# Performance work log

Hardware: AMD Instinct MI355X
Metric: run time of the kernel (lower is better)

## Reference

```python
import jax, jax.numpy as jnp
import numpy as np

EMB = 512
N_MODELS = 5
HID = 64
N_Q = 2048
N_P = 256


def setup_inputs() -> dict:
    key = jax.random.key(0)
    ks = jax.random.split(key, 6)
    return {
        "query_features": jax.random.normal(ks[0], (N_Q, EMB), dtype=jnp.float32),
        "prototypes": jax.random.normal(ks[1], (N_P, EMB), dtype=jnp.float32),
        # first Linear: weight [64, 2*EMB], bias [64], per model
        "W1": jax.random.normal(ks[2], (N_MODELS, HID, 2 * EMB), dtype=jnp.float32) * 0.02,
        "b1": jax.random.normal(ks[3], (N_MODELS, HID), dtype=jnp.float32) * 0.02,
        # second Linear: weight [1, 64] -> stored as [64], bias scalar per model
        "W2": jax.random.normal(ks[4], (N_MODELS, HID), dtype=jnp.float32) * 0.02,
        "b2": jax.random.normal(ks[5], (N_MODELS,), dtype=jnp.float32) * 0.02,
    }


def reference(query_features, prototypes, W1, b1, W2, b2):
    d = query_features.shape[1]
    # cat([q_i, p_j]) @ W1^T == q_i @ W1[:, :d]^T + p_j @ W1[:, d:]^T
    W1q = W1[:, :, :d]   # [M, H, d]
    W1p = W1[:, :, d:]   # [M, H, d]
    hq = jnp.einsum('qd,mhd->mqh', query_features, W1q)  # [M, Q, H]
    hp = jnp.einsum('pd,mhd->mph', prototypes, W1p)      # [M, P, H]
    h = jax.nn.relu(hq[:, :, None, :] + hp[:, None, :, :] + b1[:, None, None, :])  # [M, Q, P, H]
    out = jnp.einsum('mqph,mh->mqp', h, W2) + b2[:, None, None]  # [M, Q, P]
    mean_d = out.mean(axis=0)
    # torch.std default is unbiased (ddof=1)
    unc = jnp.std(out, axis=0, ddof=1)
    return mean_d * jnp.exp(-unc)
```

## Files before the change

### kernel.cpp

```cpp
#include <hip/hip_runtime.h>
#include <math.h>

#define EMB 512
#define NM 5
#define HID 64
#define NQ 2048
#define NP 256

typedef __attribute__((ext_vector_type(8))) short short8;
typedef __attribute__((ext_vector_type(4))) float floatx4;

#define A_BY 0u
#define B_BY 2621440u

#define LST 72

__device__ inline unsigned short bfr(float f) {
    unsigned u = __float_as_uint(f);
    u += 0x7FFFu + ((u >> 16) & 1u);
    return (unsigned short)(u >> 16);
}

__device__ inline void cvt8(float4 a, float4 b, short8& hi, short8& lo) {
#define C1(I, V) { unsigned short h_ = bfr(V); hi[I] = (short)h_; \
    lo[I] = (short)bfr(V - __uint_as_float(((unsigned)h_) << 16)); }
    C1(0, a.x) C1(1, a.y) C1(2, a.z) C1(3, a.w)
    C1(4, b.x) C1(5, b.y) C1(6, b.z) C1(7, b.w)
#undef C1
}
__device__ inline void cvt8hi(float4 a, float4 b, short8& hi) {
    hi[0] = (short)bfr(a.x); hi[1] = (short)bfr(a.y);
    hi[2] = (short)bfr(a.z); hi[3] = (short)bfr(a.w);
    hi[4] = (short)bfr(b.x); hi[5] = (short)bfr(b.y);
    hi[6] = (short)bfr(b.z); hi[7] = (short)bfr(b.w);
}

__global__ __launch_bounds__(256) void gemm_v3(const float* __restrict__ Q,
                                               const float* __restrict__ P,
                                               const float* __restrict__ W1,
                                               const float* __restrict__ b1,
                                               float* __restrict__ A,
                                               float* __restrict__ Bv) {
    __shared__ short XH[2][16 * LST];
    __shared__ short WH[2][64 * LST];
    __shared__ short WL[2][64 * LST];

    int tid  = threadIdx.x;
    int lane = tid & 63;
    int ht   = tid >> 6;
    int m    = blockIdx.x % 5;
    int rt   = blockIdx.x / 5;
    int r0   = rt * 16;
    bool isQ = rt < 128;

    int wrow = tid >> 3;
    int wg8  = (tid & 7) * 8;
    const float* wb  = W1 + (size_t)m * 64 * 1024 + (isQ ? 0 : EMB);
    const float* wp0 = wb + (size_t)wrow * 1024 + wg8;
    const float* wp1 = wb + (size_t)(wrow + 32) * 1024 + wg8;
    bool hasX = tid < 128;
    int xrow  = tid >> 3;
    const float* xp = (isQ ? Q + (size_t)(r0 + xrow) * EMB
                           : P + (size_t)(r0 - NQ + xrow) * EMB) + wg8;

    int arix = (lane & 15) * LST + (lane >> 4) * 8;
    int brix = (ht * 16 + (lane & 15)) * LST + (lane >> 4) * 8;

    floatx4 ac = {0, 0, 0, 0};
    float4 w00, w01, w10, w11, x0, x1;

    w00 = *(const float4*)&wp0[0]; w01 = *(const float4*)&wp0[4];
    w10 = *(const float4*)&wp1[0]; w11 = *(const float4*)&wp1[4];
    if (hasX) { x0 = *(const float4*)&xp[0]; x1 = *(const float4*)&xp[4]; }
    {
        short8 hi, lo;
        cvt8(w00, w01, hi, lo);
        *(short8*)&WH[0][wrow * LST + wg8] = hi;
        *(short8*)&WL[0][wrow * LST + wg8] = lo;
        cvt8(w10, w11, hi, lo);
        *(short8*)&WH[0][(wrow + 32) * LST + wg8] = hi;
        *(short8*)&WL[0][(wrow + 32) * LST + wg8] = lo;
        if (hasX) { short8 xh; cvt8hi(x0, x1, xh);
                    *(short8*)&XH[0][xrow * LST + wg8] = xh; }
    }

#pragma unroll 1
    for (int c = 0; c < 8; ++c) {
        int cur = c & 1;
        if (c < 7) {
            int k0 = (c + 1) * 64;
            w00 = *(const float4*)&wp0[k0]; w01 = *(const float4*)&wp0[k0 + 4];
            w10 = *(const float4*)&wp1[k0]; w11 = *(const float4*)&wp1[k0 + 4];
            if (hasX) { x0 = *(const float4*)&xp[k0]; x1 = *(const float4*)&xp[k0 + 4]; }
        }
        __syncthreads();

#pragma unroll
        for (int s = 0; s < 2; ++s) {
            short8 Ah = *(const short8*)&XH[cur][arix + s * 32];
            short8 Bh = *(const short8*)&WH[cur][brix + s * 32];
            short8 Bl = *(const short8*)&WL[cur][brix + s * 32];
            ac = __builtin_amdgcn_mfma_f32_16x16x32_bf16(Ah, Bl, ac, 0, 0, 0);
            ac = __builtin_amdgcn_mfma_f32_16x16x32_bf16(Ah, Bh, ac, 0, 0, 0);
        }

        if (c < 7) {
            int nb = cur ^ 1;
            short8 hi, lo;
            cvt8(w00, w01, hi, lo);
            *(short8*)&WH[nb][wrow * LST + wg8] = hi;
            *(short8*)&WL[nb][wrow * LST + wg8] = lo;
            cvt8(w10, w11, hi, lo);
            *(short8*)&WH[nb][(wrow + 32) * LST + wg8] = hi;
            *(short8*)&WL[nb][(wrow + 32) * LST + wg8] = lo;
            if (hasX) { short8 xh; cvt8hi(x0, x1, xh);
                        *(short8*)&XH[nb][xrow * LST + wg8] = xh; }
        }
    }

    int col  = lane & 15;
    int rloc = (lane >> 4) * 4;
    int hh   = ht * 16 + col;
    int rr   = r0 + rloc;

    if (isQ) {
        float bb = b1[m * 64 + hh];
        float* dst = &A[((size_t)m * NQ + rr) * HID + hh];
        dst[0 * HID] = ac.x + bb; dst[1 * HID] = ac.y + bb;
        dst[2 * HID] = ac.z + bb; dst[3 * HID] = ac.w + bb;
    } else {
        int p = rr - NQ;
        float* dst = &Bv[(((size_t)(m * 16 + (hh >> 2))) * NP + p) * 4 + (hh & 3)];
        dst[0 * 4] = ac.x; dst[1 * 4] = ac.y; dst[2 * 4] = ac.z; dst[3 * 4] = ac.w;
    }
}

__global__ __launch_bounds__(256) void fused_main(const float* __restrict__ A,
                                                  const float* __restrict__ Bv,
                                                  const float* __restrict__ W2,
                                                  const float* __restrict__ b2,
                                                  float* __restrict__ out) {
    int p  = threadIdx.x;
    int q0 = blockIdx.x * 2;

    float s1a = 0, s2a = 0, s1b = 0, s2b = 0;
    const float4* Bq = (const float4*)Bv + p;

#pragma unroll 1
    for (int m = 0; m < NM; ++m) {
        const float4* bm = Bq + (size_t)m * 16 * NP;
        float4 B0 = bm[0*NP],  B1 = bm[1*NP],  B2 = bm[2*NP],  B3 = bm[3*NP];
        float4 B4 = bm[4*NP],  B5 = bm[5*NP],  B6 = bm[6*NP],  B7 = bm[7*NP];
        float4 B8 = bm[8*NP],  B9 = bm[9*NP],  B10= bm[10*NP], B11= bm[11*NP];
        float4 B12= bm[12*NP], B13= bm[13*NP], B14= bm[14*NP], B15= bm[15*NP];

        const float* Ar  = A + ((size_t)m * NQ + q0) * HID;
        const float* Wp2 = W2 + m * HID;
        float oa = 0.f, ob = 0.f;

#define HSTEP(BF, H0) { \
        float wa=Wp2[H0+0], wb=Wp2[H0+1], wc=Wp2[H0+2], wd=Wp2[H0+3]; \
        oa = fmaf(fmaxf(Ar[H0+0]    + BF.x, 0.f), wa, oa); \
        oa = fmaf(fmaxf(Ar[H0+1]    + BF.y, 0.f), wb, oa); \
        oa = fmaf(fmaxf(Ar[H0+2]    + BF.z, 0.f), wc, oa); \
        oa = fmaf(fmaxf(Ar[H0+3]    + BF.w, 0.f), wd, oa); \
        ob = fmaf(fmaxf(Ar[64+H0+0] + BF.x, 0.f), wa, ob); \
        ob = fmaf(fmaxf(Ar[64+H0+1] + BF.y, 0.f), wb, ob); \
        ob = fmaf(fmaxf(Ar[64+H0+2] + BF.z, 0.f), wc, ob); \
        ob = fmaf(fmaxf(Ar[64+H0+3] + BF.w, 0.f), wd, ob); }

        HSTEP(B0,  0)  HSTEP(B1,  4)  HSTEP(B2,  8)  HSTEP(B3, 12)
        HSTEP(B4, 16)  HSTEP(B5, 20)  HSTEP(B6, 24)  HSTEP(B7, 28)
        HSTEP(B8, 32)  HSTEP(B9, 36)  HSTEP(B10,40)  HSTEP(B11,44)
        HSTEP(B12,48)  HSTEP(B13,52)  HSTEP(B14,56)  HSTEP(B15,60)
#undef HSTEP

        float bb = b2[m];
        float xa = oa + bb, xb = ob + bb;
        s1a += xa; s2a = fmaf(xa, xa, s2a);
        s1b += xb; s2b = fmaf(xb, xb, s2b);
    }

    {
        float mean = s1a * 0.2f;
        float var  = fmaxf((s2a - s1a * s1a * 0.2f) * 0.25f, 0.f);
        out[(size_t)q0 * NP + p] = mean * __expf(-sqrtf(var));
    }
    {
        float mean = s1b * 0.2f;
        float var  = fmaxf((s2b - s1b * s1b * 0.2f) * 0.25f, 0.f);
        out[(size_t)(q0 + 1) * NP + p] = mean * __expf(-sqrtf(var));
    }
}

extern "C" void kernel_launch(void* const* d_in, const int* in_sizes, int n_in,
                              void* d_out, int out_size, void* d_ws, size_t ws_size,
                              hipStream_t stream) {
    const float* Q  = (const float*)d_in[0];
    const float* P  = (const float*)d_in[1];
    const float* W1 = (const float*)d_in[2];
    const float* b1 = (const float*)d_in[3];
    const float* W2 = (const float*)d_in[4];
    const float* b2 = (const float*)d_in[5];
    float* out = (float*)d_out;

    char*  ws = (char*)d_ws;
    float* A  = (float*)(ws + A_BY);
    float* B  = (float*)(ws + B_BY);

    gemm_v3<<<720, 256, 0, stream>>>(Q, P, W1, b1, A, B);
    fused_main<<<1024, 256, 0, stream>>>(A, B, W2, b2, out);
}
```

Before: 93.16 us.

## Split projection GEMM into single-wave blocks to drop block-level barriers

The projection GEMM now launches 2880 blocks of one 64-thread wavefront each, every block computing one 16x16 output tile instead of a 16x64 tile shared by four waves. Because each block is a single wave, the __syncthreads in the double-buffered K loop is removed. The goal is to cut barrier stalls and spread the work over more blocks. The cost is that each query/prototype row tile is now loaded and converted to bf16 four times instead of once, so global loads and conversion work rise.

Result: slower. 100.1 us (+7.4%).

```diff
diff --git a/kernel.cpp b/kernel.cpp
--- a/kernel.cpp
+++ b/kernel.cpp
@@ -35,53 +35,52 @@
     hi[6] = (short)bfr(b.z); hi[7] = (short)bfr(b.w);
 }
 
-__global__ __launch_bounds__(256) void gemm_v3(const float* __restrict__ Q,
-                                               const float* __restrict__ P,
-                                               const float* __restrict__ W1,
-                                               const float* __restrict__ b1,
-                                               float* __restrict__ A,
-                                               float* __restrict__ Bv) {
+__global__ __launch_bounds__(64) void gemm_w(const float* __restrict__ Q,
+                                             const float* __restrict__ P,
+                                             const float* __restrict__ W1,
+                                             const float* __restrict__ b1,
+                                             float* __restrict__ A,
+                                             float* __restrict__ Bv) {
     __shared__ short XH[2][16 * LST];
-    __shared__ short WH[2][64 * LST];
-    __shared__ short WL[2][64 * LST];
-
-    int tid  = threadIdx.x;
-    int lane = tid & 63;
-    int ht   = tid >> 6;
-    int m    = blockIdx.x % 5;
-    int rt   = blockIdx.x / 5;
+    __shared__ short WH[2][16 * LST];
+    __shared__ short WL[2][16 * LST];
+
+    int lane = threadIdx.x;
+    int b    = blockIdx.x;
+    int ht   = b & 3;
+    int mr   = b >> 2;
+    int m    = mr % 5;
+    int rt   = mr / 5;
     int r0   = rt * 16;
     bool isQ = rt < 128;
 
-    int wrow = tid >> 3;
-    int wg8  = (tid & 7) * 8;
-    const float* wb  = W1 + (size_t)m * 64 * 1024 + (isQ ? 0 : EMB);
-    const float* wp0 = wb + (size_t)wrow * 1024 + wg8;
-    const float* wp1 = wb + (size_t)(wrow + 32) * 1024 + wg8;
-    bool hasX = tid < 128;
-    int xrow  = tid >> 3;
-    const float* xp = (isQ ? Q + (size_t)(r0 + xrow) * EMB
-                           : P + (size_t)(r0 - NQ + xrow) * EMB) + wg8;
+    int srow = lane >> 2;
+    int sk   = (lane & 3) * 16;
+    const float* xp = (isQ ? Q + (size_t)(r0 + srow) * EMB
+                           : P + (size_t)(r0 - NQ + srow) * EMB) + sk;
+    const float* wp = W1 + ((size_t)m * 64 + ht * 16 + srow) * 1024
+                      + (isQ ? 0 : EMB) + sk;
 
     int arix = (lane & 15) * LST + (lane >> 4) * 8;
-    int brix = (ht * 16 + (lane & 15)) * LST + (lane >> 4) * 8;
 
     floatx4 ac = {0, 0, 0, 0};
-    float4 w00, w01, w10, w11, x0, x1;
-
-    w00 = *(const float4*)&wp0[0]; w01 = *(const float4*)&wp0[4];
-    w10 = *(const float4*)&wp1[0]; w11 = *(const float4*)&wp1[4];
-    if (hasX) { x0 = *(const float4*)&xp[0]; x1 = *(const float4*)&xp[4]; }
+    float4 x0, x1, x2, x3, w0, w1, w2, w3;
+
+    x0 = *(const float4*)&xp[0];  x1 = *(const float4*)&xp[4];
+    x2 = *(const float4*)&xp[8];  x3 = *(const float4*)&xp[12];
+    w0 = *(const float4*)&wp[0];  w1 = *(const float4*)&wp[4];
+    w2 = *(const float4*)&wp[8];  w3 = *(const float4*)&wp[12];
     {
-        short8 hi, lo;
-        cvt8(w00, w01, hi, lo);
-        *(short8*)&WH[0][wrow * LST + wg8] = hi;
-        *(short8*)&WL[0][wrow * LST + wg8] = lo;
-        cvt8(w10, w11, hi, lo);
-        *(short8*)&WH[0][(wrow + 32) * LST + wg8] = hi;
-        *(short8*)&WL[0][(wrow + 32) * LST + wg8] = lo;
-        if (hasX) { short8 xh; cvt8hi(x0, x1, xh);
-                    *(short8*)&XH[0][xrow * LST + wg8] = xh; }
+        short8 h0, h1, hi, lo;
+        cvt8hi(x0, x1, h0); cvt8hi(x2, x3, h1);
+        *(short8*)&XH[0][srow * LST + sk] = h0;
+        *(short8*)&XH[0][srow * LST + sk + 8] = h1;
+        cvt8(w0, w1, hi, lo);
+        *(short8*)&WH[0][srow * LST + sk] = hi;
+        *(short8*)&WL[0][srow * LST + sk] = lo;
+        cvt8(w2, w3, hi, lo);
+        *(short8*)&WH[0][srow * LST + sk + 8] = hi;
+        *(short8*)&WL[0][srow * LST + sk + 8] = lo;
     }
 
 #pragma unroll 1
@@ -89,32 +88,33 @@
         int cur = c & 1;
         if (c < 7) {
             int k0 = (c + 1) * 64;
-            w00 = *(const float4*)&wp0[k0]; w01 = *(const float4*)&wp0[k0 + 4];
-            w10 = *(const float4*)&wp1[k0]; w11 = *(const float4*)&wp1[k0 + 4];
-            if (hasX) { x0 = *(const float4*)&xp[k0]; x1 = *(const float4*)&xp[k0 + 4]; }
+            x0 = *(const float4*)&xp[k0];     x1 = *(const float4*)&xp[k0 + 4];
+            x2 = *(const float4*)&xp[k0 + 8]; x3 = *(const float4*)&xp[k0 + 12];
+            w0 = *(const float4*)&wp[k0];     w1 = *(const float4*)&wp[k0 + 4];
+            w2 = *(const float4*)&wp[k0 + 8]; w3 = *(const float4*)&wp[k0 + 12];
         }
-        __syncthreads();
 
 #pragma unroll
         for (int s = 0; s < 2; ++s) {
             short8 Ah = *(const short8*)&XH[cur][arix + s * 32];
-            short8 Bh = *(const short8*)&WH[cur][brix + s * 32];
-            short8 Bl = *(const short8*)&WL[cur][brix + s * 32];
+            short8 Bh = *(const short8*)&WH[cur][arix + s * 32];
+            short8 Bl = *(const short8*)&WL[cur][arix + s * 32];
             ac = __builtin_amdgcn_mfma_f32_16x16x32_bf16(Ah, Bl, ac, 0, 0, 0);
             ac = __builtin_amdgcn_mfma_f32_16x16x32_bf16(Ah, Bh, ac, 0, 0, 0);
         }
 
         if (c < 7) {
             int nb = cur ^ 1;
-            short8 hi, lo;
-            cvt8(w00, w01, hi, lo);
-            *(short8*)&WH[nb][wrow * LST + wg8] = hi;
-            *(short8*)&WL[nb][wrow * LST + wg8] = lo;
-            cvt8(w10, w11, hi, lo);
-            *(short8*)&WH[nb][(wrow + 32) * LST + wg8] = hi;
-            *(short8*)&WL[nb][(wrow + 32) * LST + wg8] = lo;
-            if (hasX) { short8 xh; cvt8hi(x0, x1, xh);
-                        *(short8*)&XH[nb][xrow * LST + wg8] = xh; }
+            short8 h0, h1, hi, lo;
+            cvt8hi(x0, x1, h0); cvt8hi(x2, x3, h1);
+            *(short8*)&XH[nb][srow * LST + sk] = h0;
+            *(short8*)&XH[nb][srow * LST + sk + 8] = h1;
+            cvt8(w0, w1, hi, lo);
+            *(short8*)&WH[nb][srow * LST + sk] = hi;
+            *(short8*)&WL[nb][srow * LST + sk] = lo;
+            cvt8(w2, w3, hi, lo);
+            *(short8*)&WH[nb][srow * LST + sk + 8] = hi;
+            *(short8*)&WL[nb][srow * LST + sk + 8] = lo;
         }
     }
 
@@ -208,6 +208,6 @@
     float* A  = (float*)(ws + A_BY);
     float* B  = (float*)(ws + B_BY);
 
-    gemm_v3<<<720, 256, 0, stream>>>(Q, P, W1, b1, A, B);
+    gemm_w<<<2880, 64, 0, stream>>>(Q, P, W1, b1, A, B);
     fused_main<<<1024, 256, 0, stream>>>(A, B, W2, b2, out);
 }
```
